# Kernel tuning notes

Hardware: AMD Instinct MI355X
Metric: run time of the kernel (lower is better)

Reference implementation:

```python
import jax, jax.numpy as jnp
import numpy as np
import math

B, NIN, DIM, QK, GS, L, BINS = 512, 128, 512, 128, 32, 2, 100
HID = int(DIM * 2.0)
G = NIN // GS
ROT = 32  # rotary dim = min(32, query_key_dim)
EPS = 1e-5


def setup_inputs() -> dict:
    key = jax.random.key(0)
    ks = jax.random.split(key, 8)
    r = jax.random.normal
    return {
        "tokens": jax.random.randint(ks[0], (B, NIN), 0, BINS),
        "emb": r(ks[1], (NIN, BINS, DIM), jnp.float32) * 0.02,
        "pos_emb": r(ks[2], (NIN, DIM), jnp.float32) * 0.01,
        "norm_g": jnp.ones((L,), jnp.float32),
        "Wh": r(ks[3], (L, DIM, 2 * HID), jnp.float32) / math.sqrt(DIM),
        "bh": jnp.zeros((L, 2 * HID), jnp.float32),
        "Wqk": r(ks[4], (L, DIM, QK), jnp.float32) / math.sqrt(DIM),
        "bqk": jnp.zeros((L, QK), jnp.float32),
        "gamma": r(ks[5], (L, 4, QK), jnp.float32) * 0.02,
        "beta": jnp.zeros((L, 4, QK), jnp.float32),
        "rp": r(ks[6], (L, 32), jnp.float32) * 0.02,
        "Wout": r(ks[7], (L, HID, DIM), jnp.float32) / math.sqrt(HID),
        "bout": jnp.zeros((L, DIM), jnp.float32),
        "ln_g": jnp.ones((DIM,), jnp.float32),
        "ln_b": jnp.zeros((DIM,), jnp.float32),
    }


def _t5_buckets(n, num_buckets=32, max_distance=128):
    # causal T5 relative position buckets, computed statically
    pos = np.arange(n)
    rel = pos[None, :] - pos[:, None]
    neg = np.maximum(-rel, 0)
    max_exact = num_buckets // 2
    vl = max_exact + (np.log(np.maximum(neg, 1) / max_exact) / np.log(max_distance / max_exact) * (num_buckets - max_exact)).astype(np.int64)
    vl = np.minimum(vl, num_buckets - 1)
    return jnp.asarray(np.where(neg < max_exact, neg, vl))


def _rotary_cos_sin(n):
    inv = 1.0 / (10000.0 ** (np.arange(0, ROT, 2) / ROT))
    f = np.einsum('i,j->ij', np.arange(n), inv)  # [n, ROT/2]
    f = np.repeat(f, 2, axis=-1)                 # interleaved-pair freqs [n, ROT]
    return jnp.asarray(np.cos(f), jnp.float32), jnp.asarray(np.sin(f), jnp.float32)


def _apply_rotary(x, cos, sin):
    xr, xp = x[..., :ROT], x[..., ROT:]
    x2 = xr.reshape(*xr.shape[:-1], ROT // 2, 2)
    rh = jnp.stack((-x2[..., 1], x2[..., 0]), axis=-1).reshape(xr.shape)
    return jnp.concatenate([xr * cos + rh * sin, xp], axis=-1)


def reference(tokens, emb, pos_emb, norm_g, Wh, bh, Wqk, bqk, gamma, beta, rp, Wout, bout, ln_g, ln_b):
    # per-column embedding lookup + positional embedding
    x = emb[jnp.arange(NIN)[None, :], tokens] + pos_emb  # [B, NIN, DIM]
    buckets = _t5_buckets(GS)
    cos, sin = _rotary_cos_sin(NIN)
    t5_scale = QK ** 0.5
    causal_mask = jnp.triu(jnp.ones((GS, GS), bool), 1)

    def grp(t):
        return t.reshape(B, G, GS, t.shape[-1])

    def layer(h, p):
        ng, Wh_l, bh_l, Wqk_l, bqk_l, gm, bt, rp_l, Wo_l, bo_l = p
        # ScaleNorm
        nrm = jnp.linalg.norm(h, axis=-1, keepdims=True) * DIM ** -0.5
        nx = h / jnp.maximum(nrm, EPS) * ng
        # shift_tokens: shift first half of features by one position
        xs, xp = nx[..., :DIM // 2], nx[..., DIM // 2:]
        xs = jnp.pad(xs, ((0, 0), (1, 0), (0, 0)))[:, :-1]
        nx = jnp.concatenate([xs, xp], axis=-1)
        hid = jax.nn.silu(nx @ Wh_l + bh_l)
        v, gate = hid[..., :HID], hid[..., HID:]
        qk = jax.nn.silu(nx @ Wqk_l + bqk_l)
        qs = qk[..., None, :] * gm + bt  # [B, NIN, 4, QK]
        quad_q = _apply_rotary(qs[..., 0, :], cos, sin)
        lin_q = _apply_rotary(qs[..., 1, :], cos, sin)
        quad_k = _apply_rotary(qs[..., 2, :], cos, sin)
        lin_k = _apply_rotary(qs[..., 3, :], cos, sin)
        qq, lq, kk, lk, vg = map(grp, (quad_q, lin_q, quad_k, lin_k, v))
        # grouped quadratic attention with ReLU^2 attn fn and T5 rel-pos bias
        sim = jnp.einsum('bgid,bgjd->bgij', qq, kk) / GS + rp_l[buckets] * t5_scale
        attn = jnp.square(jax.nn.relu(sim))
        attn = jnp.where(causal_mask, 0.0, attn)
        quad_out = jnp.einsum('bgij,bgje->bgie', attn, vg)
        # causal linear attention across groups (shifted cumsum of kv stats)
        lin_kv = jnp.einsum('bgnd,bgne->bgde', lk, vg) / GS
        lin_kv = jnp.cumsum(lin_kv, axis=1)
        lin_kv = jnp.pad(lin_kv, ((0, 0), (1, 0), (0, 0), (0, 0)))[:, :-1]
        lin_out = jnp.einsum('bgde,bgnd->bgne', lin_kv, lq)
        out = gate * (quad_out + lin_out).reshape(B, NIN, HID)
        return out @ Wo_l + bo_l + h, None

    x, _ = jax.lax.scan(layer, x, (norm_g, Wh, bh, Wqk, bqk, gamma, beta, rp, Wout, bout))
    mu = x.mean(-1, keepdims=True)
    var = x.var(-1, keepdims=True)
    return (x - mu) / jnp.sqrt(var + EPS) * ln_g + ln_b
```

## Files before the change

kernel.cpp:

```cpp
#include <hip/hip_runtime.h>
#include <hip/hip_bf16.h>
#include <math.h>
#include <stdint.h>

#define BB   512
#define NIN  128
#define DIMD 512
#define QKD  128
#define GSZ  32
#define GRP  4
#define HID  1024
#define HID2 2048
#define NFUSE 2176
#define ROT  32
#define NLAYER 2
#define EPSF 1e-5f
#define BINS 100

typedef __bf16 bf16x8 __attribute__((ext_vector_type(8)));
typedef float  f32x4  __attribute__((ext_vector_type(4)));
typedef float  f32x16 __attribute__((ext_vector_type(16)));

__device__ __forceinline__ unsigned short f2bf(float f) {
    union { float f; uint32_t u; } v; v.f = f;
    return (unsigned short)((v.u + 0x7FFFu + ((v.u >> 16) & 1u)) >> 16);
}
__device__ __forceinline__ float bf2f(unsigned short h) {
    union { uint32_t u; float f; } v; v.u = ((uint32_t)h) << 16;
    return v.f;
}

__global__ void k_embed(const int* __restrict__ tokens, const float* __restrict__ emb,
                        const float* __restrict__ pos, float* __restrict__ h) {
    int bn = blockIdx.x;
    int n  = bn % NIN;
    int tok = tokens[bn];
    const float4* e4 = (const float4*)(emb + ((size_t)n * BINS + tok) * DIMD);
    const float4* p4 = (const float4*)(pos + (size_t)n * DIMD);
    float4* h4 = (float4*)(h + (size_t)bn * DIMD);
    int t = threadIdx.x;
    float4 a = e4[t], b = p4[t];
    h4[t] = make_float4(a.x + b.x, a.y + b.y, a.z + b.z, a.w + b.w);
}

__global__ void k_nxf(const float* __restrict__ h, unsigned short* __restrict__ nx,
                      const float* __restrict__ ngp) {
    int bn = blockIdx.x; int n = bn % NIN;
    int t = threadIdx.x;
    float4 v = ((const float4*)(h + (size_t)bn * DIMD))[t];
    float sq = v.x * v.x + v.y * v.y + v.z * v.z + v.w * v.w;
    __shared__ float red[2];
    #pragma unroll
    for (int o = 32; o; o >>= 1) sq += __shfl_down(sq, o);
    int lane = t & 63, w = t >> 6;
    if (lane == 0) red[w] = sq;
    __syncthreads();
    float s = red[0] + red[1];
    float nrm = sqrtf(s) * (1.0f / sqrtf((float)DIMD));
    float sc = ngp[0] / fmaxf(nrm, EPSF);
    ushort4 o = make_ushort4(f2bf(v.x * sc), f2bf(v.y * sc), f2bf(v.z * sc), f2bf(v.w * sc));
    if (t < 64) {
        if (n == 0)
            ((ushort4*)(nx + (size_t)bn * DIMD))[t] = make_ushort4(0, 0, 0, 0);
        if (n != NIN - 1)
            ((ushort4*)(nx + (size_t)(bn + 1) * DIMD))[t] = o;
    } else {
        ((ushort4*)(nx + (size_t)bn * DIMD))[t] = o;
    }
}

__global__ void k_wcast(const float* __restrict__ W, unsigned short* __restrict__ Wt,
                        int K, int N) {
    int idx = blockIdx.x * 256 + threadIdx.x;
    int total = N * (K / 8);
    if (idx >= total) return;
    int kb = idx / N, n = idx % N;
    #pragma unroll
    for (int j = 0; j < 8; ++j)
        Wt[(size_t)n * K + kb * 8 + j] = f2bf(W[(size_t)(kb * 8 + j) * N + n]);
}

#define GLOAD_LDS(gp, lp) __builtin_amdgcn_global_load_lds( \
    (const __attribute__((address_space(1))) uint32_t*)(gp), \
    (__attribute__((address_space(3))) uint32_t*)(lp), 16, 0, 0)

__global__ __launch_bounds__(256) void k_gemm_f(
        const unsigned short* __restrict__ A,
        const unsigned short* __restrict__ Bt,
        const float* __restrict__ bias0,
        const float* __restrict__ bias1,
        float* __restrict__ Cf,
        unsigned short* __restrict__ vTp,
        unsigned short* __restrict__ gatep,
        int M, int N, int K) {
    __shared__ unsigned short As[2][128 * 32];
    __shared__ unsigned short Bs[2][128 * 32];
    const int tid = threadIdx.x;

    int flat = blockIdx.y * gridDim.x + blockIdx.x;
    int nwg  = gridDim.x * gridDim.y;
    int q = nwg >> 3, r = nwg & 7;
    int xcd = flat & 7, idx = flat >> 3;
    int swz = (xcd < r ? xcd * (q + 1) : r * (q + 1) + (xcd - r) * q) + idx;
    const int bxi = swz % gridDim.x, byi = swz / gridDim.x;
    const int bm = byi * 128, bn = bxi * 128;

    const int lane = tid & 63, wave = tid >> 6;
    const int wm = (wave >> 1) * 64, wn = (wave & 1) * 64;
    const int l15 = lane & 15, l4 = lane >> 4;

    f32x4 acc[4][4];
    #pragma unroll
    for (int i = 0; i < 4; ++i)
        #pragma unroll
        for (int j = 0; j < 4; ++j) acc[i][j] = (f32x4){0.f, 0.f, 0.f, 0.f};

    const int rowA = tid >> 2;
    const int colB = (tid & 3) * 16;
    const char* gA = (const char*)(A  + (size_t)(bm + rowA) * K) + colB;
    const char* gB = (const char*)(Bt + (size_t)(bn + rowA) * K) + colB;
    const size_t stride64 = (size_t)64 * K * 2;

    #define STAGEF(bi, k0) do { \
        const char* sA_ = gA + (size_t)(k0) * 2; \
        const char* sB_ = gB + (size_t)(k0) * 2; \
        GLOAD_LDS(sA_,            &As[bi][tid * 8]); \
        GLOAD_LDS(sA_ + stride64, &As[bi][tid * 8 + 2048]); \
        GLOAD_LDS(sB_,            &Bs[bi][tid * 8]); \
        GLOAD_LDS(sB_ + stride64, &Bs[bi][tid * 8 + 2048]); \
    } while (0)

    const int NIT = K / 32;
    STAGEF(0, 0);
    STAGEF(1, 32);

    for (int t = 0; t < NIT; ++t) {
        const int cur = t & 1;
        if (t + 1 < NIT) asm volatile("s_waitcnt vmcnt(4)" ::: "memory");
        else             asm volatile("s_waitcnt vmcnt(0)" ::: "memory");
        __builtin_amdgcn_s_barrier();
        __builtin_amdgcn_sched_barrier(0);

        bf16x8 af[4], bfr[4];
        #pragma unroll
        for (int f = 0; f < 4; ++f) {
            af[f]  = *(const bf16x8*)&As[cur][(wm + f * 16 + l15) * 32 + l4 * 8];
            bfr[f] = *(const bf16x8*)&Bs[cur][(wn + f * 16 + l15) * 32 + l4 * 8];
        }
        asm volatile("s_waitcnt lgkmcnt(0)" ::: "memory");
        __builtin_amdgcn_sched_barrier(0);
        __builtin_amdgcn_s_barrier();
        __builtin_amdgcn_sched_barrier(0);
        if (t + 2 < NIT) STAGEF(cur, (t + 2) * 32);

        #pragma unroll
        for (int i = 0; i < 4; ++i)
            #pragma unroll
            for (int j = 0; j < 4; ++j)
                acc[i][j] = __builtin_amdgcn_mfma_f32_16x16x32_bf16(af[i], bfr[j], acc[i][j], 0, 0, 0);
    }
    #undef STAGEF

    #pragma unroll
    for (int i = 0; i < 4; ++i) {
        const int n0 = wm + i * 16 + l4 * 4;
        #pragma unroll
        for (int j = 0; j < 4; ++j) {
            const int col = bn + wn + j * 16 + l15;
            float bsv = (col < 2 * HID) ? bias0[col] : bias1[col - 2 * HID];
            float vv[4];
            #pragma unroll
            for (int rr = 0; rr < 4; ++rr) {
                float v = acc[i][j][rr] + bsv;
                vv[rr] = v / (1.0f + __expf(-v));
            }
            if (col < HID) {
                ushort4 o = make_ushort4(f2bf(vv[0]), f2bf(vv[1]), f2bf(vv[2]), f2bf(vv[3]));
                *(ushort4*)&vTp[((size_t)byi * HID + col) * NIN + n0] = o;
            } else if (col < 2 * HID) {
                #pragma unroll
                for (int rr = 0; rr < 4; ++rr)
                    gatep[(size_t)(bm + n0 + rr) * HID + (col - HID)] = f2bf(vv[rr]);
            } else {
                #pragma unroll
                for (int rr = 0; rr < 4; ++rr)
                    Cf[(size_t)(bm + n0 + rr) * QKD + (col - 2 * HID)] = vv[rr];
            }
        }
    }
}

__global__ __launch_bounds__(256, 2) void k_gemm_o(
        const unsigned short* __restrict__ A,
        const unsigned short* __restrict__ Bt,
        const float* __restrict__ bias0,
        const float* __restrict__ resid,
        float* __restrict__ Cf,
        int M, int N, int K) {
    __shared__ unsigned short As[2][256 * 32];
    __shared__ unsigned short Bs[2][128 * 32];
    const int tid = threadIdx.x;

    int flat = blockIdx.y * gridDim.x + blockIdx.x;
    int nwg  = gridDim.x * gridDim.y;
    int q = nwg >> 3, r = nwg & 7;
    int xcd = flat & 7, idx = flat >> 3;
    int swz = (xcd < r ? xcd * (q + 1) : r * (q + 1) + (xcd - r) * q) + idx;
    const int bxi = swz % gridDim.x, byi = swz / gridDim.x;
    const int bm = byi * 256, bn = bxi * 128;

    const int lane = tid & 63, wave = tid >> 6;
    const int l15 = lane & 15, l4 = lane >> 4;

    f32x4 acc[4][8];
    #pragma unroll
    for (int i = 0; i < 4; ++i)
        #pragma unroll
        for (int j = 0; j < 8; ++j) acc[i][j] = (f32x4){0.f, 0.f, 0.f, 0.f};

    const int rowA = tid >> 2;
    const int colO = (tid & 3) * 16;
    const int colS = colO ^ ((rowA & 3) << 4);
    const char* gA = (const char*)(A  + (size_t)(bm + rowA) * K) + colS;
    const char* gB = (const char*)(Bt + (size_t)(bn + rowA) * K) + colS;
    const size_t stride64 = (size_t)64 * K * 2;
    unsigned short* dA0 = &As[0][tid * 8];
    unsigned short* dA1 = &As[1][tid * 8];
    unsigned short* dB0 = &Bs[0][tid * 8];
    unsigned short* dB1 = &Bs[1][tid * 8];

    #define STAGE2(dA, dB, k0) do { \
        const char* sA_ = gA + (size_t)(k0) * 2; \
        const char* sB_ = gB + (size_t)(k0) * 2; \
        GLOAD_LDS(sA_,                 (dA)); \
        GLOAD_LDS(sA_ +     stride64,  (dA) + 2048); \
        GLOAD_LDS(sA_ + 2 * stride64,  (dA) + 4096); \
        GLOAD_LDS(sA_ + 3 * stride64,  (dA) + 6144); \
        GLOAD_LDS(sB_,                 (dB)); \
        GLOAD_LDS(sB_ +     stride64,  (dB) + 2048); \
    } while (0)

    STAGE2(dA0, dB0, 0);
    asm volatile("s_waitcnt vmcnt(0)" ::: "memory");
    __syncthreads();

    const int NIT = K / 32;
    int bufc = 0;
    for (int it = 0; it < NIT; ++it) {
        if (it + 1 < NIT) {
            if (bufc == 0) STAGE2(dA1, dB1, (it + 1) * 32);
            else           STAGE2(dA0, dB0, (it + 1) * 32);
        }
        const unsigned short* Ab = As[bufc];
        const unsigned short* Bb = Bs[bufc];
        bf16x8 af[4], bfr[8];
        #pragma unroll
        for (int f = 0; f < 4; ++f) {
            int rA = wave * 64 + f * 16 + l15;
            af[f] = *(const bf16x8*)&Ab[rA * 32 + ((l4 ^ (rA & 3)) << 3)];
        }
        #pragma unroll
        for (int c = 0; c < 8; ++c) {
            int rB = c * 16 + l15;
            bfr[c] = *(const bf16x8*)&Bb[rB * 32 + ((l4 ^ (rB & 3)) << 3)];
        }
        #pragma unroll
        for (int f = 0; f < 4; ++f)
            #pragma unroll
            for (int c = 0; c < 8; ++c)
                acc[f][c] = __builtin_amdgcn_mfma_f32_16x16x32_bf16(af[f], bfr[c], acc[f][c], 0, 0, 0);
        asm volatile("s_waitcnt vmcnt(0)" ::: "memory");
        __syncthreads();
        bufc ^= 1;
    }
    #undef STAGE2

    #pragma unroll
    for (int f = 0; f < 4; ++f) {
        const int n0 = wave * 64 + f * 16 + l4 * 4;
        #pragma unroll
        for (int c = 0; c < 8; ++c) {
            const int col = bn + c * 16 + l15;
            float bsv = bias0[col];
            #pragma unroll
            for (int rr = 0; rr < 4; ++rr) {
                size_t row = bm + n0 + rr;
                Cf[row * N + col] = acc[f][c][rr] + bsv + resid[row * N + col];
            }
        }
    }
}

__global__ void k_cossin(float* __restrict__ cosb, float* __restrict__ sinb) {
    int idx = blockIdx.x * 256 + threadIdx.x;
    if (idx >= NIN * 16) return;
    int n = idx / 16, i = idx % 16;
    double inv = pow(10000.0, -(double)(2 * i) / (double)ROT);
    double f = (double)n * inv;
    cosb[idx] = (float)cos(f);
    sinb[idx] = (float)sin(f);
}

__global__ void k_rot(const float* __restrict__ qk, const float* __restrict__ gm,
                      const float* __restrict__ bt, const float* __restrict__ cosb,
                      const float* __restrict__ sinb, unsigned short* __restrict__ q4) {
    int bn = blockIdx.x; int n = bn % NIN;
    int d = threadIdx.x;
    float x = qk[(size_t)bn * QKD + d];
    float xp0 = 0.f;
    int dp = d ^ 1;
    if (d < ROT) xp0 = qk[(size_t)bn * QKD + dp];
    #pragma unroll
    for (int c = 0; c < 4; ++c) {
        float val = x * gm[c * QKD + d] + bt[c * QKD + d];
        float outv;
        if (d < ROT) {
            int i = d >> 1;
            float cs = cosb[n * 16 + i], sn = sinb[n * 16 + i];
            float xp = xp0 * gm[c * QKD + dp] + bt[c * QKD + dp];
            outv = ((d & 1) == 0) ? (val * cs - xp * sn) : (val * cs + xp * sn);
        } else outv = val;
        q4[((size_t)bn * 4 + c) * QKD + d] = f2bf(outv);
    }
}

__global__ __launch_bounds__(256) void k_attn2(
        const unsigned short* __restrict__ q4,
        const unsigned short* __restrict__ gatep,
        const unsigned short* __restrict__ vT,
        const float* __restrict__ rp,
        unsigned short* __restrict__ attn_out) {
    int et = blockIdx.x, b = blockIdx.y;
    int tid = threadIdx.x, wave = tid >> 6, lane = tid & 63;
    int l31 = lane & 31, lhi = lane >> 5;

    __shared__ unsigned short S[32][136];
    __shared__ float rps_d[32];
    if (tid < 32) {
        int d = tid, bucket;
        if (d < 16) bucket = d;
        else {
            bucket = 16 + (int)(logf((float)d * (1.0f / 16.0f)) * (16.0f / logf(8.0f)));
            if (bucket > 31) bucket = 31;
        }
        rps_d[tid] = rp[bucket] * sqrtf((float)QKD);
    }
    __syncthreads();

    size_t bbase = (size_t)b * NIN;
    int e0 = et * 256 + wave * 64;
    const unsigned short* vbase = vT + (size_t)b * HID * NIN;

    for (int g = 0; g < GRP; ++g) {
        if (wave <= g) {
            int gp = wave;
            bool quad = (gp == g);
            const unsigned short* Qb = q4 + ((bbase + g  * 32 + l31) * 4 + (quad ? 0 : 1)) * QKD;
            const unsigned short* Kb = q4 + ((bbase + gp * 32 + l31) * 4 + (quad ? 2 : 3)) * QKD;
            f32x16 sa = {};
            #pragma unroll
            for (int kk = 0; kk < 8; ++kk) {
                bf16x8 aq = *(const bf16x8*)(Qb + kk * 16 + lhi * 8);
                bf16x8 bk = *(const bf16x8*)(Kb + kk * 16 + lhi * 8);
                sa = __builtin_amdgcn_mfma_f32_32x32x16_bf16(aq, bk, sa, 0, 0, 0);
            }
            int j = l31;
            #pragma unroll
            for (int r = 0; r < 16; ++r) {
                int i = (r & 3) + 8 * (r >> 2) + 4 * lhi;
                float s = sa[r] * (1.0f / GSZ);
                if (quad) {
                    if (j > i) s = 0.f;
                    else {
                        s += rps_d[i - j];
                        s = fmaxf(s, 0.f);
                        s = s * s;
                    }
                }
                S[i][gp * 32 + j] = f2bf(s);
            }
        }
        __syncthreads();

        f32x16 o0 = {}, o1 = {};
        int KT = 2 * (g + 1);
        for (int kk = 0; kk < KT; ++kk) {
            int k0 = kk * 16 + lhi * 8;
            bf16x8 af = *(const bf16x8*)&S[l31][k0];
            bf16x8 b0 = *(const bf16x8*)(vbase + (size_t)(e0 + l31) * NIN + k0);
            bf16x8 b1 = *(const bf16x8*)(vbase + (size_t)(e0 + 32 + l31) * NIN + k0);
            o0 = __builtin_amdgcn_mfma_f32_32x32x16_bf16(af, b0, o0, 0, 0, 0);
            o1 = __builtin_amdgcn_mfma_f32_32x32x16_bf16(af, b1, o1, 0, 0, 0);
        }
        __syncthreads();

        int ea = e0 + l31, eb = e0 + 32 + l31;
        #pragma unroll
        for (int r = 0; r < 16; ++r) {
            int i = (r & 3) + 8 * (r >> 2) + 4 * lhi;
            size_t row = bbase + g * 32 + i;
            float ga = bf2f(gatep[row * HID + ea]);
            float gb = bf2f(gatep[row * HID + eb]);
            attn_out[row * HID + ea] = f2bf(ga * o0[r]);
            attn_out[row * HID + eb] = f2bf(gb * o1[r]);
        }
    }
}

__global__ void k_ln(const float* __restrict__ h, const float* __restrict__ lng,
                     const float* __restrict__ lnb, float* __restrict__ out) {
    int bn = blockIdx.x;
    int t = threadIdx.x;
    const float4* r4 = (const float4*)(h + (size_t)bn * DIMD);
    float4 v = r4[t];
    float s  = v.x + v.y + v.z + v.w;
    float sq = v.x * v.x + v.y * v.y + v.z * v.z + v.w * v.w;
    __shared__ float red[4];
    #pragma unroll
    for (int o = 32; o; o >>= 1) { s += __shfl_down(s, o); sq += __shfl_down(sq, o); }
    int lane = t & 63, w = t >> 6;
    if (lane == 0) { red[w] = s; red[2 + w] = sq; }
    __syncthreads();
    float mu  = (red[0] + red[1]) * (1.0f / DIMD);
    float var = (red[2] + red[3]) * (1.0f / DIMD) - mu * mu;
    float rstd = 1.0f / sqrtf(var + EPSF);
    float4 gg = ((const float4*)lng)[t];
    float4 bb = ((const float4*)lnb)[t];
    float4 o;
    o.x = (v.x - mu) * rstd * gg.x + bb.x;
    o.y = (v.y - mu) * rstd * gg.y + bb.y;
    o.z = (v.z - mu) * rstd * gg.z + bb.z;
    o.w = (v.w - mu) * rstd * gg.w + bb.w;
    ((float4*)(out + (size_t)bn * DIMD))[t] = o;
}

extern "C" void kernel_launch(void* const* d_in, const int* in_sizes, int n_in,
                              void* d_out, int out_size, void* d_ws, size_t ws_size,
                              hipStream_t stream) {
    const int*   tokens = (const int*)d_in[0];
    const float* emb    = (const float*)d_in[1];
    const float* pos    = (const float*)d_in[2];
    const float* norm_g = (const float*)d_in[3];
    const float* Wh     = (const float*)d_in[4];
    const float* bh     = (const float*)d_in[5];
    const float* Wqk    = (const float*)d_in[6];
    const float* bqk    = (const float*)d_in[7];
    const float* gamma  = (const float*)d_in[8];
    const float* beta   = (const float*)d_in[9];
    const float* rp     = (const float*)d_in[10];
    const float* Wout   = (const float*)d_in[11];
    const float* bout   = (const float*)d_in[12];
    const float* lng    = (const float*)d_in[13];
    const float* lnb    = (const float*)d_in[14];

    float* h  = (float*)d_out;
    float* ws = (float*)d_ws;

    size_t off = 0;
    float* cosb  = ws + off; off += NIN * 16;
    float* sinb  = ws + off; off += NIN * 16;
    unsigned short* whqkT = (unsigned short*)(ws + off); off += (size_t)NLAYER * NFUSE * DIMD / 2;
    unsigned short* woutT = (unsigned short*)(ws + off); off += (size_t)NLAYER * DIMD * HID / 2;
    off = (off + 63) & ~(size_t)63;
    const size_t fixedFloats = off;

    const size_t wsFloats = ws_size / sizeof(float);
    const size_t perBatch = (size_t)NIN * (DIMD / 2 + HID / 2 + HID / 2 + QKD + DIMD / 2 + HID / 2);
    int CB = BB;
    while (CB > 2 && fixedFloats + (size_t)CB * perBatch + 64 > wsFloats) CB >>= 1;

    unsigned short* nx    = (unsigned short*)(ws + off); off += (size_t)CB * NIN * DIMD / 2;
    unsigned short* vT    = (unsigned short*)(ws + off); off += (size_t)CB * HID * NIN / 2;
    unsigned short* gateB = (unsigned short*)(ws + off); off += (size_t)CB * NIN * HID / 2;
    float*          qk    = ws + off;                    off += (size_t)CB * NIN * QKD;
    unsigned short* q4    = (unsigned short*)(ws + off); off += (size_t)CB * NIN * DIMD / 2;
    unsigned short* attnB = (unsigned short*)(ws + off); off += (size_t)CB * NIN * HID / 2;

    const int BN_ = BB * NIN;

    k_cossin<<<8, 256, 0, stream>>>(cosb, sinb);
    k_embed<<<BN_, 128, 0, stream>>>(tokens, emb, pos, h);

    for (int l = 0; l < NLAYER; ++l) {
        unsigned short* whqkT_l = whqkT + (size_t)l * NFUSE * DIMD;
        k_wcast<<<(HID2 * DIMD / 8 + 255) / 256, 256, 0, stream>>>(
            Wh + (size_t)l * DIMD * HID2,  whqkT_l, DIMD, HID2);
        k_wcast<<<(QKD * DIMD / 8 + 255) / 256, 256, 0, stream>>>(
            Wqk + (size_t)l * DIMD * QKD,  whqkT_l + (size_t)HID2 * DIMD, DIMD, QKD);
        k_wcast<<<(DIMD * HID / 8 + 255) / 256, 256, 0, stream>>>(
            Wout + (size_t)l * HID * DIMD, woutT + (size_t)l * DIMD * HID, HID, DIMD);
    }

    for (int l = 0; l < NLAYER; ++l) {
        const float* bh_l  = bh   + (size_t)l * HID2;
        const float* bqk_l = bqk  + (size_t)l * QKD;
        const float* gm_l  = gamma+ (size_t)l * 4 * QKD;
        const float* bt_l  = beta + (size_t)l * 4 * QKD;
        const float* rp_l  = rp   + (size_t)l * 32;
        const float* bo_l  = bout + (size_t)l * DIMD;
        const unsigned short* whqkT_l = whqkT + (size_t)l * NFUSE * DIMD;
        const unsigned short* woutT_l = woutT + (size_t)l * DIMD * HID;

        for (int c0 = 0; c0 < BB; c0 += CB) {
            const int rowsC = CB * NIN;
            float* h_c = h + (size_t)c0 * NIN * DIMD;

            k_nxf<<<rowsC, 128, 0, stream>>>(h_c, nx, norm_g + l);

            dim3 g1(NFUSE / 128, rowsC / 128);
            k_gemm_f<<<g1, 256, 0, stream>>>(nx, whqkT_l, bh_l, bqk_l,
                                             qk, vT, gateB, rowsC, NFUSE, DIMD);

            k_rot<<<rowsC, 128, 0, stream>>>(qk, gm_l, bt_l, cosb, sinb, q4);

            dim3 ga(HID / 256, CB);
            k_attn2<<<ga, 256, 0, stream>>>(q4, gateB, vT, rp_l, attnB);

            dim3 g3(DIMD / 128, rowsC / 256);
            k_gemm_o<<<g3, 256, 0, stream>>>(attnB, woutT_l, bo_l, h_c, h_c,
                                             rowsC, DIMD, HID);
        }
    }

    k_ln<<<BN_, 128, 0, stream>>>(h, lng, lnb, (float*)d_out);
}
```

Before: 1.348 ms.

## Deepen GEMM load pipelines: triple-buffer fused GEMM, prefetch-two in output GEMM

The fused input-projection GEMM moves from double to triple LDS buffering with three stages in flight, waiting on vmcnt(8). The output GEMM is restructured to match: two stages are issued up front, and each iteration waits on a partial vmcnt, reads fragments, then barriers before refilling the freed buffer, instead of waiting for all loads to finish every iteration. Both MFMA loops are wrapped in s_setprio to favour math issue. The aim is to hide global-load latency, at the cost of more LDS per block, which may lower occupancy.

```diff
diff --git a/kernel.cpp b/kernel.cpp
--- a/kernel.cpp
+++ b/kernel.cpp
@@ -93,8 +93,8 @@
         unsigned short* __restrict__ vTp,
         unsigned short* __restrict__ gatep,
         int M, int N, int K) {
-    __shared__ unsigned short As[2][128 * 32];
-    __shared__ unsigned short Bs[2][128 * 32];
+    __shared__ unsigned short As[3][128 * 32];
+    __shared__ unsigned short Bs[3][128 * 32];
     const int tid = threadIdx.x;
 
     int flat = blockIdx.y * gridDim.x + blockIdx.x;
@@ -133,11 +133,14 @@
     const int NIT = K / 32;
     STAGEF(0, 0);
     STAGEF(1, 32);
-
+    STAGEF(2, 64);
+
+    int cur = 0;
     for (int t = 0; t < NIT; ++t) {
-        const int cur = t & 1;
-        if (t + 1 < NIT) asm volatile("s_waitcnt vmcnt(4)" ::: "memory");
-        else             asm volatile("s_waitcnt vmcnt(0)" ::: "memory");
+        const int rem = NIT - 1 - t;
+        if (rem >= 2)      asm volatile("s_waitcnt vmcnt(8)" ::: "memory");
+        else if (rem == 1) asm volatile("s_waitcnt vmcnt(4)" ::: "memory");
+        else               asm volatile("s_waitcnt vmcnt(0)" ::: "memory");
         __builtin_amdgcn_s_barrier();
         __builtin_amdgcn_sched_barrier(0);
 
@@ -151,13 +154,17 @@
         __builtin_amdgcn_sched_barrier(0);
         __builtin_amdgcn_s_barrier();
         __builtin_amdgcn_sched_barrier(0);
-        if (t + 2 < NIT) STAGEF(cur, (t + 2) * 32);
-
+        if (t + 3 < NIT) STAGEF(cur, (t + 3) * 32);
+
+        __builtin_amdgcn_s_setprio(1);
         #pragma unroll
         for (int i = 0; i < 4; ++i)
             #pragma unroll
             for (int j = 0; j < 4; ++j)
                 acc[i][j] = __builtin_amdgcn_mfma_f32_16x16x32_bf16(af[i], bfr[j], acc[i][j], 0, 0, 0);
+        __builtin_amdgcn_s_setprio(0);
+
+        cur = (cur == 2) ? 0 : cur + 1;
     }
     #undef STAGEF
 
@@ -224,56 +231,55 @@
     const char* gA = (const char*)(A  + (size_t)(bm + rowA) * K) + colS;
     const char* gB = (const char*)(Bt + (size_t)(bn + rowA) * K) + colS;
     const size_t stride64 = (size_t)64 * K * 2;
-    unsigned short* dA0 = &As[0][tid * 8];
-    unsigned short* dA1 = &As[1][tid * 8];
-    unsigned short* dB0 = &Bs[0][tid * 8];
-    unsigned short* dB1 = &Bs[1][tid * 8];
-
-    #define STAGE2(dA, dB, k0) do { \
+
+    #define STAGEO(bi, k0) do { \
         const char* sA_ = gA + (size_t)(k0) * 2; \
         const char* sB_ = gB + (size_t)(k0) * 2; \
-        GLOAD_LDS(sA_,                 (dA)); \
-        GLOAD_LDS(sA_ +     stride64,  (dA) + 2048); \
-        GLOAD_LDS(sA_ + 2 * stride64,  (dA) + 4096); \
-        GLOAD_LDS(sA_ + 3 * stride64,  (dA) + 6144); \
-        GLOAD_LDS(sB_,                 (dB)); \
-        GLOAD_LDS(sB_ +     stride64,  (dB) + 2048); \
+        GLOAD_LDS(sA_,                 &As[bi][tid * 8]); \
+        GLOAD_LDS(sA_ +     stride64,  &As[bi][tid * 8 + 2048]); \
+        GLOAD_LDS(sA_ + 2 * stride64,  &As[bi][tid * 8 + 4096]); \
+        GLOAD_LDS(sA_ + 3 * stride64,  &As[bi][tid * 8 + 6144]); \
+        GLOAD_LDS(sB_,                 &Bs[bi][tid * 8]); \
+        GLOAD_LDS(sB_ +     stride64,  &Bs[bi][tid * 8 + 2048]); \
     } while (0)
 
-    STAGE2(dA0, dB0, 0);
-    asm volatile("s_waitcnt vmcnt(0)" ::: "memory");
-    __syncthreads();
-
     const int NIT = K / 32;
-    int bufc = 0;
-    for (int it = 0; it < NIT; ++it) {
-        if (it + 1 < NIT) {
-            if (bufc == 0) STAGE2(dA1, dB1, (it + 1) * 32);
-            else           STAGE2(dA0, dB0, (it + 1) * 32);
-        }
-        const unsigned short* Ab = As[bufc];
-        const unsigned short* Bb = Bs[bufc];
+    STAGEO(0, 0);
+    STAGEO(1, 32);
+
+    for (int t = 0; t < NIT; ++t) {
+        const int cur = t & 1;
+        if (t + 1 < NIT) asm volatile("s_waitcnt vmcnt(6)" ::: "memory");
+        else             asm volatile("s_waitcnt vmcnt(0)" ::: "memory");
+        __builtin_amdgcn_s_barrier();
+        __builtin_amdgcn_sched_barrier(0);
+
         bf16x8 af[4], bfr[8];
         #pragma unroll
         for (int f = 0; f < 4; ++f) {
             int rA = wave * 64 + f * 16 + l15;
-            af[f] = *(const bf16x8*)&Ab[rA * 32 + ((l4 ^ (rA & 3)) << 3)];
+            af[f] = *(const bf16x8*)&As[cur][rA * 32 + ((l4 ^ (rA & 3)) << 3)];
         }
         #pragma unroll
         for (int c = 0; c < 8; ++c) {
             int rB = c * 16 + l15;
-            bfr[c] = *(const bf16x8*)&Bb[rB * 32 + ((l4 ^ (rB & 3)) << 3)];
-        }
+            bfr[c] = *(const bf16x8*)&Bs[cur][rB * 32 + ((l4 ^ (rB & 3)) << 3)];
+        }
+        asm volatile("s_waitcnt lgkmcnt(0)" ::: "memory");
+        __builtin_amdgcn_sched_barrier(0);
+        __builtin_amdgcn_s_barrier();
+        __builtin_amdgcn_sched_barrier(0);
+        if (t + 2 < NIT) STAGEO(cur, (t + 2) * 32);
+
+        __builtin_amdgcn_s_setprio(1);
         #pragma unroll
         for (int f = 0; f < 4; ++f)
             #pragma unroll
             for (int c = 0; c < 8; ++c)
                 acc[f][c] = __builtin_amdgcn_mfma_f32_16x16x32_bf16(af[f], bfr[c], acc[f][c], 0, 0, 0);
-        asm volatile("s_waitcnt vmcnt(0)" ::: "memory");
-        __syncthreads();
-        bufc ^= 1;
-    }
-    #undef STAGE2
+        __builtin_amdgcn_s_setprio(0);
+    }
+    #undef STAGEO
 
     #pragma unroll
     for (int f = 0; f < 4; ++f) {
```

Measured after the change: 1.349 ms. About the same (+0.1%).
